# Performance work log

Hardware: AMD Instinct MI355X
Metric: run time of the kernel (lower is better)

## Reference

```python
import jax, jax.numpy as jnp
import numpy as np

N_CLASSES = 5
N_SAMPLES = 512
D_EMB = 512


def setup_inputs() -> dict:
    key = jax.random.key(0)
    k1, k2, k3 = jax.random.split(key, 3)
    prediction = jax.random.normal(k1, (N_SAMPLES, D_EMB), dtype=jnp.float32)
    target = jax.random.randint(k2, (N_SAMPLES,), 0, N_CLASSES)
    # learnable_map=None -> all learnable, init = inverse_softplus(0.5 + 0.5*U[0,1))
    t = 0.5 + 0.5 * jax.random.uniform(k3, (N_CLASSES - 1,), dtype=jnp.float32)
    distances_raw = jnp.log(jnp.exp(t) - 1.0)  # inverse softplus (t < 20 always)
    return {"prediction": prediction, "distances_raw": distances_raw, "target": target}


def reference(prediction, distances_raw, target):
    n = prediction.shape[0]
    eps = 1e-8  # torch F.cosine_similarity eps
    xn = prediction / jnp.maximum(jnp.linalg.norm(prediction, axis=1, keepdims=True), eps)
    cos = xn @ xn.T  # [i, j] pairwise cosine similarity

    same = target[:, None] == target[None, :]          # label_diff <= 0
    positives = same & ~jnp.eye(n, dtype=bool)          # same label, not self
    negatives = ~same                                   # different label

    # ordinal class positions from softplus-parameterized gaps
    pos_d = jax.nn.softplus(distances_raw)
    class_pos = jnp.concatenate([jnp.zeros(1, dtype=pos_d.dtype), jnp.cumsum(pos_d)])
    cp = class_pos[target]
    margins = jnp.where(negatives, jnp.abs(cp[:, None] - cp[None, :]), 0.0)  # [i, j]

    # Original loop over anchor-positive columns k:
    #   n_pair_loss[k][i, j] = -cos[i, k] + cos[i, j] + margins[i, j]
    #   valid iff positives[i, k] and negatives[i, j]; invalid -> relu(-inf)=0
    base = cos + margins                                # [i, j]
    diff = base[:, None, :] - cos[:, :, None]           # [i, k, j]
    val = jnp.where(negatives[:, None, :], jax.nn.relu(diff), 0.0)
    s = jnp.where(positives, val.sum(axis=2), 0.0)      # [i, k]
    negcount = negatives.sum(axis=1)                    # [i]
    cnt = jnp.where(positives, negcount[:, None], 0)    # loss_mask2
    L = s / jnp.maximum(cnt, 1)                         # per (anchor i, positive k)

    # mean over nonzero entries (mean_n_pair_loss[mean_n_pair_loss != 0].mean())
    nz = (L != 0.0).sum()
    return L.sum() / jnp.maximum(nz, 1).astype(L.dtype)
```

## Files before the change

### kernel.cpp

```cpp
#include <hip/hip_runtime.h>
#include <math.h>

#define NS 512
#define DE 512
#define NCL 5
#define NBLK 256


__global__ __launch_bounds__(512, 2) void k_all(const float* __restrict__ pred,
                                                const int* __restrict__ target,
                                                const float* __restrict__ draw,
                                                float* __restrict__ psum,
                                                int* __restrict__ pnz) {
    const int b = blockIdx.x;
    const int tid = threadIdx.x;
    const int iA = b, iB = b + 256;

    __shared__ float  rn_s[NS];
    __shared__ float  ckA[NS], ckB[NS];
    __shared__ float4 v4sA[NS / 4], v4sB[NS / 4];
    __shared__ int    pkA[NS], pkB[NS];
    __shared__ float  spart[NS * 17];
    __shared__ float  wf[8];
    __shared__ int    wi[8];
    __shared__ unsigned int pcA, pcB;

    if (tid == 0) { pcA = 0u; pcB = 0u; }

    const int w = tid >> 6, lane = tid & 63;
    const int g = lane >> 4, s = lane & 15;

    const float4* pA = (const float4*)&pred[(size_t)iA * DE];
    const float4* pB = (const float4*)&pred[(size_t)iB * DE];
    float4 fA[8], fB[8];
#pragma unroll
    for (int p = 0; p < 8; p++) { fA[p] = pA[p * 16 + s]; fB[p] = pB[p * 16 + s]; }

    const float4* p4 = (const float4*)pred;
    const float4* rj0 = p4 + (size_t)(w * 64 + g) * (DE / 4);
    const int rstep = 4 * (DE / 4);
    float4 x0[8], x1[8];
#pragma unroll
    for (int p = 0; p < 8; p++) x0[p] = rj0[p * 16 + s];
#pragma unroll
    for (int p = 0; p < 8; p++) x1[p] = rj0[rstep + p * 16 + s];

#pragma unroll
    for (int t = 0; t < 16; t++) {
        float4 xn[8];
        if (t < 14) {
            const float4* rjn = rj0 + (size_t)(t + 2) * rstep;
#pragma unroll
            for (int p = 0; p < 8; p++) xn[p] = rjn[p * 16 + s];
        }
        const int j = w * 64 + t * 4 + g;
        float aA = 0.0f, aB = 0.0f, aS = 0.0f;
#pragma unroll
        for (int p = 0; p < 8; p++) {
            float4 x = x0[p];
            aA = fmaf(x.x, fA[p].x, aA); aA = fmaf(x.y, fA[p].y, aA);
            aA = fmaf(x.z, fA[p].z, aA); aA = fmaf(x.w, fA[p].w, aA);
            aB = fmaf(x.x, fB[p].x, aB); aB = fmaf(x.y, fB[p].y, aB);
            aB = fmaf(x.z, fB[p].z, aB); aB = fmaf(x.w, fB[p].w, aB);
            aS = fmaf(x.x, x.x, aS);     aS = fmaf(x.y, x.y, aS);
            aS = fmaf(x.z, x.z, aS);     aS = fmaf(x.w, x.w, aS);
        }
#pragma unroll
        for (int m = 1; m <= 8; m <<= 1) {
            aA += __shfl_xor(aA, m);
            aB += __shfl_xor(aB, m);
            aS += __shfl_xor(aS, m);
        }
        if (s == 0) {
            ckA[j] = aA;
            ckB[j] = aB;
            rn_s[j] = 1.0f / fmaxf(sqrtf(aS), 1e-8f);
        }
#pragma unroll
        for (int p = 0; p < 8; p++) { x0[p] = x1[p]; x1[p] = xn[p]; }
    }

    float cp[NCL];
    cp[0] = 0.0f;
#pragma unroll
    for (int c = 0; c < NCL - 1; c++) cp[c + 1] = cp[c] + log1pf(expf(draw[c]));
    const int tiA = target[iA], tiB = target[iB];
    const float cpA = cp[tiA], cpB = cp[tiB];
    const int j = tid;
    const int tj = target[j];
    const float cpj = cp[tj];
    __syncthreads();

    const float rniA = rn_s[iA], rniB = rn_s[iB], rnj = rn_s[j];
    int nc;
    {
        float c0 = ckA[j] * rniA * rnj;
        bool n0 = (tj != tiA);
        ckA[j] = c0;
        ((float*)v4sA)[j] = n0 ? (c0 + fabsf(cpA - cpj)) : -1e30f;
        if (!n0 && j != iA) pkA[atomicAdd(&pcA, 1u)] = j;
        nc = (n0 ? 1 : 0);
    }
    {
        float c0 = ckB[j] * rniB * rnj;
        bool n0 = (tj != tiB);
        ckB[j] = c0;
        ((float*)v4sB)[j] = n0 ? (c0 + fabsf(cpB - cpj)) : -1e30f;
        if (!n0 && j != iB) pkB[atomicAdd(&pcB, 1u)] = j;
        nc += (n0 ? 1 : 0) << 16;
    }
#pragma unroll
    for (int m = 1; m <= 32; m <<= 1) nc += __shfl_xor(nc, m);
    if ((tid & 63) == 0) wi[tid >> 6] = nc;
    __syncthreads();
    int negpack = 0;
#pragma unroll
    for (int q = 0; q < 8; q++) negpack += wi[q];
    const int negA = negpack & 0xffff;
    const int negB = negpack >> 16;
    const unsigned int nposA = pcA, nposB = pcB;

    const int kl = tid & 31, jc = tid >> 5;
    const float denA = (float)(negA > 1 ? negA : 1);
    const float denB = (float)(negB > 1 ? negB : 1);
    float contrib = 0.0f;
    int nzc = 0;

    {
        float4 vj[8];
#pragma unroll
        for (int t = 0; t < 8; t++) vj[t] = v4sA[jc * 8 + t];
        for (unsigned int p = kl; p < nposA; p += 32) {
            const float ckp = ckA[pkA[p]];
            float s0 = 0.0f, s1 = 0.0f;
#pragma unroll
            for (int t = 0; t < 8; t++) {
                float4 wv = vj[t];
                s0 += fmaxf(wv.x - ckp, 0.0f) + fmaxf(wv.y - ckp, 0.0f);
                s1 += fmaxf(wv.z - ckp, 0.0f) + fmaxf(wv.w - ckp, 0.0f);
            }
            spart[p * 17 + jc] = s0 + s1;
        }
        __syncthreads();
        for (unsigned int p = tid; p < nposA; p += 512) {
            float s0 = 0.0f;
#pragma unroll
            for (int q = 0; q < 16; q++) s0 += spart[p * 17 + q];
            contrib += s0 / denA;
            if (s0 != 0.0f) nzc++;
        }
        __syncthreads();
    }
    {
        float4 vj[8];
#pragma unroll
        for (int t = 0; t < 8; t++) vj[t] = v4sB[jc * 8 + t];
        for (unsigned int p = kl; p < nposB; p += 32) {
            const float ckp = ckB[pkB[p]];
            float s0 = 0.0f, s1 = 0.0f;
#pragma unroll
            for (int t = 0; t < 8; t++) {
                float4 wv = vj[t];
                s0 += fmaxf(wv.x - ckp, 0.0f) + fmaxf(wv.y - ckp, 0.0f);
                s1 += fmaxf(wv.z - ckp, 0.0f) + fmaxf(wv.w - ckp, 0.0f);
            }
            spart[p * 17 + jc] = s0 + s1;
        }
        __syncthreads();
        for (unsigned int p = tid; p < nposB; p += 512) {
            float s0 = 0.0f;
#pragma unroll
            for (int q = 0; q < 16; q++) s0 += spart[p * 17 + q];
            contrib += s0 / denB;
            if (s0 != 0.0f) nzc++;
        }
    }

#pragma unroll
    for (int m = 1; m <= 32; m <<= 1) {
        contrib += __shfl_xor(contrib, m);
        nzc     += __shfl_xor(nzc, m);
    }
    __syncthreads();
    if ((tid & 63) == 0) { wf[tid >> 6] = contrib; wi[tid >> 6] = nzc; }
    __syncthreads();
    if (tid == 0) {
        float sfin = 0.0f; int nfin = 0;
#pragma unroll
        for (int q = 0; q < 8; q++) { sfin += wf[q]; nfin += wi[q]; }
        psum[b] = sfin;
        pnz[b]  = nfin;
    }
}

__global__ __launch_bounds__(256) void k_final(const float* __restrict__ psum,
                                               const int* __restrict__ pnz,
                                               float* __restrict__ out) {
    const int tid = threadIdx.x;
    __shared__ float rf[256];
    __shared__ int   ri[256];
    rf[tid] = psum[tid];
    ri[tid] = pnz[tid];
    __syncthreads();
    for (int s = 128; s > 0; s >>= 1) {
        if (tid < s) { rf[tid] += rf[tid + s]; ri[tid] += ri[tid + s]; }
        __syncthreads();
    }
    if (tid == 0) {
        int n = ri[0];
        out[0] = rf[0] / (float)(n > 1 ? n : 1);
    }
}

extern "C" void kernel_launch(void* const* d_in, const int* in_sizes, int n_in,
                              void* d_out, int out_size, void* d_ws, size_t ws_size,
                              hipStream_t stream) {
    const float* pred   = (const float*)d_in[0];
    const float* draw   = (const float*)d_in[1];
    const int*   target = (const int*)d_in[2];
    float* out = (float*)d_out;

    float* psum = (float*)d_ws;
    int*   pnz  = (int*)(psum + NBLK);

    hipLaunchKernelGGL(k_all, dim3(NBLK), dim3(512), 0, stream,
                       pred, target, draw, psum, pnz);
    hipLaunchKernelGGL(k_final, dim3(1), dim3(256), 0, stream, psum, pnz, out);
}
```

Baseline: 76.37 us.

## Split Gram matrix computation into a separate register-tiled kernel

Moves the cosine-similarity computation out of the fused per-anchor kernel into a dedicated kernel. Each block there computes an 8-row by 128-column tile of the normalized Gram matrix and writes it to workspace. The loss kernel then reads its two anchor rows from that matrix. Before, each block streamed all 512 rows of the prediction matrix to serve only 2 anchors; now each streamed row serves 8 anchors. The cost is an extra kernel launch and a 1 MB round trip through global memory for the cosine matrix.

```diff
diff --git a/kernel.cpp b/kernel.cpp
--- a/kernel.cpp
+++ b/kernel.cpp
@@ -7,16 +7,101 @@
 #define NBLK 256
 
 
-__global__ __launch_bounds__(512, 2) void k_all(const float* __restrict__ pred,
-                                                const int* __restrict__ target,
-                                                const float* __restrict__ draw,
-                                                float* __restrict__ psum,
-                                                int* __restrict__ pnz) {
+__global__ __launch_bounds__(512, 2) void k_gram(const float* __restrict__ pred,
+                                                 float* __restrict__ cosmat) {
+    const int b  = blockIdx.x;
+    const int ga = b >> 2;
+    const int q  = b & 3;
+    const int a0 = ga * 8;
+    const int j0 = q * 128;
+
+    const int tid  = threadIdx.x;
+    const int w    = tid >> 6, lane = tid & 63;
+    const int g    = lane >> 5;
+    const int s    = lane & 31;
+
+    const float4* p4 = (const float4*)pred;
+
+    float4 fr[8][4];
+#pragma unroll
+    for (int a = 0; a < 8; a++) {
+        const float4* pa = p4 + (size_t)(a0 + a) * (DE / 4);
+#pragma unroll
+        for (int p = 0; p < 4; p++) fr[a][p] = pa[p * 32 + s];
+    }
+
+    float rnA[8];
+#pragma unroll
+    for (int a = 0; a < 8; a++) {
+        float aS = 0.0f;
+#pragma unroll
+        for (int p = 0; p < 4; p++) {
+            float4 x = fr[a][p];
+            aS = fmaf(x.x, x.x, aS); aS = fmaf(x.y, x.y, aS);
+            aS = fmaf(x.z, x.z, aS); aS = fmaf(x.w, x.w, aS);
+        }
+#pragma unroll
+        for (int m = 1; m <= 16; m <<= 1) aS += __shfl_xor(aS, m);
+        rnA[a] = 1.0f / fmaxf(sqrtf(aS), 1e-8f);
+    }
+
+    const float4* rj0 = p4 + (size_t)(j0 + w * 16 + g) * (DE / 4);
+    const int rstep = 2 * (DE / 4);
+    float4 x0[4], x1[4];
+#pragma unroll
+    for (int p = 0; p < 4; p++) x0[p] = rj0[p * 32 + s];
+#pragma unroll
+    for (int p = 0; p < 4; p++) x1[p] = rj0[rstep + p * 32 + s];
+
+#pragma unroll
+    for (int t = 0; t < 8; t++) {
+        float4 xn[4];
+        if (t < 6) {
+            const float4* rjn = rj0 + (size_t)(t + 2) * rstep;
+#pragma unroll
+            for (int p = 0; p < 4; p++) xn[p] = rjn[p * 32 + s];
+        }
+        float acc[9];
+#pragma unroll
+        for (int a = 0; a < 9; a++) acc[a] = 0.0f;
+#pragma unroll
+        for (int p = 0; p < 4; p++) {
+            float4 x = x0[p];
+            acc[8] = fmaf(x.x, x.x, acc[8]); acc[8] = fmaf(x.y, x.y, acc[8]);
+            acc[8] = fmaf(x.z, x.z, acc[8]); acc[8] = fmaf(x.w, x.w, acc[8]);
+#pragma unroll
+            for (int a = 0; a < 8; a++) {
+                float4 f = fr[a][p];
+                acc[a] = fmaf(x.x, f.x, acc[a]); acc[a] = fmaf(x.y, f.y, acc[a]);
+                acc[a] = fmaf(x.z, f.z, acc[a]); acc[a] = fmaf(x.w, f.w, acc[a]);
+            }
+        }
+#pragma unroll
+        for (int m = 1; m <= 16; m <<= 1) {
+#pragma unroll
+            for (int a = 0; a < 9; a++) acc[a] += __shfl_xor(acc[a], m);
+        }
+        if (s == 0) {
+            const int jj = j0 + w * 16 + t * 2 + g;
+            const float rnj = 1.0f / fmaxf(sqrtf(acc[8]), 1e-8f);
+#pragma unroll
+            for (int a = 0; a < 8; a++)
+                cosmat[(size_t)(a0 + a) * NS + jj] = acc[a] * rnA[a] * rnj;
+        }
+#pragma unroll
+        for (int p = 0; p < 4; p++) { x0[p] = x1[p]; x1[p] = xn[p]; }
+    }
+}
+
+__global__ __launch_bounds__(512, 2) void k_loss(const float* __restrict__ cosmat,
+                                                 const int* __restrict__ target,
+                                                 const float* __restrict__ draw,
+                                                 float* __restrict__ psum,
+                                                 int* __restrict__ pnz) {
     const int b = blockIdx.x;
     const int tid = threadIdx.x;
     const int iA = b, iB = b + 256;
 
-    __shared__ float  rn_s[NS];
     __shared__ float  ckA[NS], ckB[NS];
     __shared__ float4 v4sA[NS / 4], v4sB[NS / 4];
     __shared__ int    pkA[NS], pkB[NS];
@@ -27,58 +112,9 @@
 
     if (tid == 0) { pcA = 0u; pcB = 0u; }
 
-    const int w = tid >> 6, lane = tid & 63;
-    const int g = lane >> 4, s = lane & 15;
-
-    const float4* pA = (const float4*)&pred[(size_t)iA * DE];
-    const float4* pB = (const float4*)&pred[(size_t)iB * DE];
-    float4 fA[8], fB[8];
-#pragma unroll
-    for (int p = 0; p < 8; p++) { fA[p] = pA[p * 16 + s]; fB[p] = pB[p * 16 + s]; }
-
-    const float4* p4 = (const float4*)pred;
-    const float4* rj0 = p4 + (size_t)(w * 64 + g) * (DE / 4);
-    const int rstep = 4 * (DE / 4);
-    float4 x0[8], x1[8];
-#pragma unroll
-    for (int p = 0; p < 8; p++) x0[p] = rj0[p * 16 + s];
-#pragma unroll
-    for (int p = 0; p < 8; p++) x1[p] = rj0[rstep + p * 16 + s];
-
-#pragma unroll
-    for (int t = 0; t < 16; t++) {
-        float4 xn[8];
-        if (t < 14) {
-            const float4* rjn = rj0 + (size_t)(t + 2) * rstep;
-#pragma unroll
-            for (int p = 0; p < 8; p++) xn[p] = rjn[p * 16 + s];
-        }
-        const int j = w * 64 + t * 4 + g;
-        float aA = 0.0f, aB = 0.0f, aS = 0.0f;
-#pragma unroll
-        for (int p = 0; p < 8; p++) {
-            float4 x = x0[p];
-            aA = fmaf(x.x, fA[p].x, aA); aA = fmaf(x.y, fA[p].y, aA);
-            aA = fmaf(x.z, fA[p].z, aA); aA = fmaf(x.w, fA[p].w, aA);
-            aB = fmaf(x.x, fB[p].x, aB); aB = fmaf(x.y, fB[p].y, aB);
-            aB = fmaf(x.z, fB[p].z, aB); aB = fmaf(x.w, fB[p].w, aB);
-            aS = fmaf(x.x, x.x, aS);     aS = fmaf(x.y, x.y, aS);
-            aS = fmaf(x.z, x.z, aS);     aS = fmaf(x.w, x.w, aS);
-        }
-#pragma unroll
-        for (int m = 1; m <= 8; m <<= 1) {
-            aA += __shfl_xor(aA, m);
-            aB += __shfl_xor(aB, m);
-            aS += __shfl_xor(aS, m);
-        }
-        if (s == 0) {
-            ckA[j] = aA;
-            ckB[j] = aB;
-            rn_s[j] = 1.0f / fmaxf(sqrtf(aS), 1e-8f);
-        }
-#pragma unroll
-        for (int p = 0; p < 8; p++) { x0[p] = x1[p]; x1[p] = xn[p]; }
-    }
+    const int j = tid;
+    const float cA = cosmat[(size_t)iA * NS + j];
+    const float cB = cosmat[(size_t)iB * NS + j];
 
     float cp[NCL];
     cp[0] = 0.0f;
@@ -86,26 +122,22 @@
     for (int c = 0; c < NCL - 1; c++) cp[c + 1] = cp[c] + log1pf(expf(draw[c]));
     const int tiA = target[iA], tiB = target[iB];
     const float cpA = cp[tiA], cpB = cp[tiB];
-    const int j = tid;
     const int tj = target[j];
     const float cpj = cp[tj];
     __syncthreads();
 
-    const float rniA = rn_s[iA], rniB = rn_s[iB], rnj = rn_s[j];
     int nc;
     {
-        float c0 = ckA[j] * rniA * rnj;
         bool n0 = (tj != tiA);
-        ckA[j] = c0;
-        ((float*)v4sA)[j] = n0 ? (c0 + fabsf(cpA - cpj)) : -1e30f;
+        ckA[j] = cA;
+        ((float*)v4sA)[j] = n0 ? (cA + fabsf(cpA - cpj)) : -1e30f;
         if (!n0 && j != iA) pkA[atomicAdd(&pcA, 1u)] = j;
         nc = (n0 ? 1 : 0);
     }
     {
-        float c0 = ckB[j] * rniB * rnj;
         bool n0 = (tj != tiB);
-        ckB[j] = c0;
-        ((float*)v4sB)[j] = n0 ? (c0 + fabsf(cpB - cpj)) : -1e30f;
+        ckB[j] = cB;
+        ((float*)v4sB)[j] = n0 ? (cB + fabsf(cpB - cpj)) : -1e30f;
         if (!n0 && j != iB) pkB[atomicAdd(&pcB, 1u)] = j;
         nc += (n0 ? 1 : 0) << 16;
     }
@@ -220,10 +252,12 @@
     const int*   target = (const int*)d_in[2];
     float* out = (float*)d_out;
 
-    float* psum = (float*)d_ws;
-    int*   pnz  = (int*)(psum + NBLK);
-
-    hipLaunchKernelGGL(k_all, dim3(NBLK), dim3(512), 0, stream,
-                       pred, target, draw, psum, pnz);
+    float* cosmat = (float*)d_ws;
+    float* psum   = cosmat + (size_t)NS * NS;
+    int*   pnz    = (int*)(psum + NBLK);
+
+    hipLaunchKernelGGL(k_gram, dim3(NBLK), dim3(512), 0, stream, pred, cosmat);
+    hipLaunchKernelGGL(k_loss, dim3(NBLK), dim3(512), 0, stream,
+                       cosmat, target, draw, psum, pnz);
     hipLaunchKernelGGL(k_final, dim3(1), dim3(256), 0, stream, psum, pnz, out);
 }
```

New measurement: 81.78 us. 7.1% more time.
